# Kernel optimization log

Measured on AMD Instinct MI355X. Metric: run time of the kernel, lower is better.

## Reference

```python
import jax, jax.numpy as jnp
import numpy as np

K = 5  # top-k neighbors, from init kwarg

def setup_inputs() -> dict:
    key = jax.random.key(0)
    k1, k2 = jax.random.split(key)
    x = jax.random.normal(k1, (16384, 256), dtype=jnp.float32)
    reference_points = jax.random.normal(k2, (100, 256), dtype=jnp.float32)
    return {"x": x, "reference_points": reference_points}

def reference(x, reference_points):
    # Faithful to tf.norm(inputs[:,None] - ref[None], axis=-1):
    # materializes the [B, P, D] difference like the original, then L2 norm.
    diff = x[:, None, :] - reference_points[None, :, :]      # [B, P, D]
    distances = jnp.sqrt(jnp.sum(diff * diff, axis=-1))      # [B, P]
    # tf.math.top_k(-distances, k) -> indices of k smallest distances
    _, indices = jax.lax.top_k(-distances, K)                # [B, K] int32
    return indices
```

## Files before the change

kernel.cpp:

```cpp
#include <hip/hip_runtime.h>
#include <float.h>
#include <math.h>

#define NREF 100
#define NREF_PAD 128
#define DIM 256
#define K 5
#define ROWS 32
#define BLOCK 128
#define LDS_DW_REF 4096

__shared__ float lds_buf[20480];

__device__ __forceinline__ int swz(int dw) { return dw ^ ((dw >> 8) & 0x1C); }

__global__ __launch_bounds__(BLOCK, 1) void knn_kernel(
    const float* __restrict__ x, const float* __restrict__ ref,
    int* __restrict__ out, int nrows) {
#pragma clang fp contract(off)
  float* lds = lds_buf;
  const int tid = threadIdx.x;
  const int tx = tid & 15;
  const int ty = tid >> 4;
  const int RB = blockIdx.x * ROWS;

  float part[4][8], t01[4][8], t45[4][8], ae[4][8], ao[4][8];

  const int xlin0 = (4 * ty) * 128;
  const int rlin0 = LDS_DW_REF + (tx * 8) * 128;
  const int xkey = (xlin0 >> 8) & 0x1C;
  const int rkey = (rlin0 >> 8) & 0x1C;

#pragma unroll 1
  for (int c = 0; c < 2; c++) {
    const int DB = c * 128;
    if (c) __syncthreads();
#pragma unroll
    for (int k = 0; k < 8; k++) {
      const int idx = tid + k * BLOCK;
      const int row = idx >> 5, dp4 = idx & 31;
      float4 v = make_float4(0.f, 0.f, 0.f, 0.f);
      if (RB + row < nrows)
        v = *reinterpret_cast<const float4*>(x + (size_t)(RB + row) * DIM + DB + dp4 * 4);
      const int t = dp4 >> 1;
      const int jp0 = (dp4 & 1) << 1;
      const int dwA = row * 128 + jp0 * 32 + 2 * t;
      *reinterpret_cast<float2*>(&lds[swz(dwA)]) = make_float2(v.x, v.y);
      *reinterpret_cast<float2*>(&lds[swz(dwA + 32)]) = make_float2(v.z, v.w);
    }
#pragma unroll
    for (int k = 0; k < 32; k++) {
      const int idx = tid + k * BLOCK;
      const int r = idx >> 5, dp4 = idx & 31;
      if (r < NREF) {
        const float4 v = *reinterpret_cast<const float4*>(ref + (size_t)r * DIM + DB + dp4 * 4);
        const int t = dp4 >> 1;
        const int jp0 = (dp4 & 1) << 1;
        const int dwA = LDS_DW_REF + r * 128 + jp0 * 32 + 2 * t;
        *reinterpret_cast<float2*>(&lds[swz(dwA)]) = make_float2(v.x, v.y);
        *reinterpret_cast<float2*>(&lds[swz(dwA + 32)]) = make_float2(v.z, v.w);
      }
    }
    __syncthreads();

#pragma unroll
    for (int jp = 0; jp < 4; jp++) {
#pragma unroll
      for (int i = 0; i < 4; i++)
#pragma unroll
        for (int rr = 0; rr < 8; rr++) { ae[i][rr] = 0.f; ao[i][rr] = 0.f; }
#pragma unroll 1
      for (int tt = 0; tt < 8; tt++) {
        const int xa = (xlin0 + jp * 32) + ((4 * tt) ^ xkey);
        const int ra = (rlin0 + jp * 32) + ((4 * tt) ^ rkey);
        float4 xv[4], rv[8];
#pragma unroll
        for (int i = 0; i < 4; i++)
          xv[i] = *reinterpret_cast<const float4*>(&lds[xa + i * 128]);
#pragma unroll
        for (int rr = 0; rr < 8; rr++)
          rv[rr] = *reinterpret_cast<const float4*>(&lds[ra + rr * 128]);
#pragma unroll
        for (int i = 0; i < 4; i++)
#pragma unroll
          for (int rr = 0; rr < 8; rr++) {
            float d0 = xv[i].x - rv[rr].x; float s0 = d0 * d0; ae[i][rr] = ae[i][rr] + s0;
            float d1 = xv[i].z - rv[rr].z; float s1 = d1 * d1; ae[i][rr] = ae[i][rr] + s1;
            float d2 = xv[i].y - rv[rr].y; float s2 = d2 * d2; ao[i][rr] = ao[i][rr] + s2;
            float d3 = xv[i].w - rv[rr].w; float s3 = d3 * d3; ao[i][rr] = ao[i][rr] + s3;
          }
      }
#pragma unroll
      for (int i = 0; i < 4; i++)
#pragma unroll
        for (int rr = 0; rr < 8; rr++) {
          const float s = ae[i][rr] + ao[i][rr];
          if (jp == 0) t01[i][rr] = s;
          else if (jp == 1) t01[i][rr] = t01[i][rr] + s;
          else if (jp == 2) t45[i][rr] = s;
          else {
            t45[i][rr] = t45[i][rr] + s;
            const float blk = t01[i][rr] + t45[i][rr];
            part[i][rr] = c ? (part[i][rr] + blk) : blk;
          }
        }
    }
  }
  __syncthreads();
#pragma unroll
  for (int i = 0; i < 4; i++)
#pragma unroll
    for (int rr = 0; rr < 8; rr++)
      lds[(4 * ty + i) * 129 + tx * 8 + rr] = sqrtf(part[i][rr]);
  __syncthreads();
  if (tid < ROWS && RB + tid < nrows) {
    float best[K]; int bidx[K];
#pragma unroll
    for (int k = 0; k < K; k++) { best[k] = FLT_MAX; bidx[k] = 0; }
    for (int r = 0; r < NREF; r++) {
      const float kv = lds[tid * 129 + r];
      if (kv < best[K - 1]) {
        int pos = K - 1;
        while (pos > 0 && kv < best[pos - 1]) {
          best[pos] = best[pos - 1]; bidx[pos] = bidx[pos - 1]; pos--;
        }
        best[pos] = kv; bidx[pos] = r;
      }
    }
    int* o = out + (size_t)(RB + tid) * K;
#pragma unroll
    for (int k = 0; k < K; k++) o[k] = bidx[k];
  }
}

extern "C" void kernel_launch(void* const* d_in, const int* in_sizes, int n_in,
                              void* d_out, int out_size, void* d_ws, size_t ws_size,
                              hipStream_t stream) {
  const float* x = (const float*)d_in[0];
  const float* ref = (const float*)d_in[1];
  int* out = (int*)d_out;
  const int nrows = in_sizes[0] / DIM;
  const int grid = (nrows + ROWS - 1) / ROWS;
  knn_kernel<<<grid, BLOCK, 0, stream>>>(x, ref, out, nrows);
}
```

Measured before the change: 128.1 us.

## Halve rows per block, use padded 64-dim LDS chunks, raise occupancy

Rows per block go from 32 to 16, and the feature dimension is staged in four 64-wide chunks in a padded (stride 68) LDS layout. This replaces the XOR-swizzled 128-wide layout. Launch bounds now allow two blocks per SM, and the accumulation uses eight independent partial sums per output in place of the nested pair tree. The goal is more blocks and more latency hiding, at the cost of more barriers, reloading the reference set twice as often per row, and a changed summation order. Row-bounds checks on loads and on the final top-k were dropped, which assumes nrows is a multiple of 16.

Result: slower. 155.3 us (+21.2%).

```diff
diff --git a/kernel.cpp b/kernel.cpp
--- a/kernel.cpp
+++ b/kernel.cpp
@@ -3,122 +3,127 @@
 #include <math.h>
 
 #define NREF 100
-#define NREF_PAD 128
 #define DIM 256
 #define K 5
-#define ROWS 32
+#define ROWS 16
 #define BLOCK 128
-#define LDS_DW_REF 4096
+#define W 68
+#define REF_OFF (ROWS * W)
+#define NREFP 128
+#define LDS_DW (REF_OFF + NREFP * W)
 
-__shared__ float lds_buf[20480];
-
-__device__ __forceinline__ int swz(int dw) { return dw ^ ((dw >> 8) & 0x1C); }
-
-__global__ __launch_bounds__(BLOCK, 1) void knn_kernel(
+__global__ __launch_bounds__(BLOCK, 2) void knn_kernel(
     const float* __restrict__ x, const float* __restrict__ ref,
     int* __restrict__ out, int nrows) {
 #pragma clang fp contract(off)
-  float* lds = lds_buf;
+  __shared__ float lds[LDS_DW];
   const int tid = threadIdx.x;
   const int tx = tid & 15;
   const int ty = tid >> 4;
   const int RB = blockIdx.x * ROWS;
 
-  float part[4][8], t01[4][8], t45[4][8], ae[4][8], ao[4][8];
+  float acc[8][2][8];
+  float part[2][8];
+#pragma unroll
+  for (int q = 0; q < 8; q++)
+#pragma unroll
+    for (int i = 0; i < 2; i++)
+#pragma unroll
+      for (int rr = 0; rr < 8; rr++) acc[q][i][rr] = 0.f;
 
-  const int xlin0 = (4 * ty) * 128;
-  const int rlin0 = LDS_DW_REF + (tx * 8) * 128;
-  const int xkey = (xlin0 >> 8) & 0x1C;
-  const int rkey = (rlin0 >> 8) & 0x1C;
+  const float* xb = &lds[2 * ty * W];
+  const float* rb = &lds[REF_OFF + tx * W];
 
 #pragma unroll 1
-  for (int c = 0; c < 2; c++) {
-    const int DB = c * 128;
+  for (int c = 0; c < 4; c++) {
+    const int DB = c * 64;
     if (c) __syncthreads();
 #pragma unroll
-    for (int k = 0; k < 8; k++) {
+    for (int k = 0; k < 2; k++) {
       const int idx = tid + k * BLOCK;
-      const int row = idx >> 5, dp4 = idx & 31;
-      float4 v = make_float4(0.f, 0.f, 0.f, 0.f);
-      if (RB + row < nrows)
-        v = *reinterpret_cast<const float4*>(x + (size_t)(RB + row) * DIM + DB + dp4 * 4);
-      const int t = dp4 >> 1;
-      const int jp0 = (dp4 & 1) << 1;
-      const int dwA = row * 128 + jp0 * 32 + 2 * t;
-      *reinterpret_cast<float2*>(&lds[swz(dwA)]) = make_float2(v.x, v.y);
-      *reinterpret_cast<float2*>(&lds[swz(dwA + 32)]) = make_float2(v.z, v.w);
+      const int row = idx >> 4, dp = (idx & 15) << 2;
+      const float4 v = *reinterpret_cast<const float4*>(
+          x + (size_t)(RB + row) * DIM + DB + dp);
+      *reinterpret_cast<float4*>(&lds[row * W + dp]) = v;
     }
 #pragma unroll
-    for (int k = 0; k < 32; k++) {
+    for (int k = 0; k < 13; k++) {
       const int idx = tid + k * BLOCK;
-      const int r = idx >> 5, dp4 = idx & 31;
+      const int r = idx >> 4, dp = (idx & 15) << 2;
       if (r < NREF) {
-        const float4 v = *reinterpret_cast<const float4*>(ref + (size_t)r * DIM + DB + dp4 * 4);
-        const int t = dp4 >> 1;
-        const int jp0 = (dp4 & 1) << 1;
-        const int dwA = LDS_DW_REF + r * 128 + jp0 * 32 + 2 * t;
-        *reinterpret_cast<float2*>(&lds[swz(dwA)]) = make_float2(v.x, v.y);
-        *reinterpret_cast<float2*>(&lds[swz(dwA + 32)]) = make_float2(v.z, v.w);
+        const float4 v = *reinterpret_cast<const float4*>(
+            ref + (size_t)r * DIM + DB + dp);
+        *reinterpret_cast<float4*>(&lds[REF_OFF + r * W + dp]) = v;
       }
     }
     __syncthreads();
-
+#pragma unroll 2
+    for (int tt = 0; tt < 8; tt++) {
+      const int d0 = tt << 3;
+      {
+        float4 xv[2], rv[8];
 #pragma unroll
-    for (int jp = 0; jp < 4; jp++) {
-#pragma unroll
-      for (int i = 0; i < 4; i++)
-#pragma unroll
-        for (int rr = 0; rr < 8; rr++) { ae[i][rr] = 0.f; ao[i][rr] = 0.f; }
-#pragma unroll 1
-      for (int tt = 0; tt < 8; tt++) {
-        const int xa = (xlin0 + jp * 32) + ((4 * tt) ^ xkey);
-        const int ra = (rlin0 + jp * 32) + ((4 * tt) ^ rkey);
-        float4 xv[4], rv[8];
-#pragma unroll
-        for (int i = 0; i < 4; i++)
-          xv[i] = *reinterpret_cast<const float4*>(&lds[xa + i * 128]);
+        for (int i = 0; i < 2; i++)
+          xv[i] = *reinterpret_cast<const float4*>(xb + i * W + d0);
 #pragma unroll
         for (int rr = 0; rr < 8; rr++)
-          rv[rr] = *reinterpret_cast<const float4*>(&lds[ra + rr * 128]);
+          rv[rr] = *reinterpret_cast<const float4*>(rb + rr * 16 * W + d0);
 #pragma unroll
-        for (int i = 0; i < 4; i++)
+        for (int i = 0; i < 2; i++)
 #pragma unroll
           for (int rr = 0; rr < 8; rr++) {
-            float d0 = xv[i].x - rv[rr].x; float s0 = d0 * d0; ae[i][rr] = ae[i][rr] + s0;
-            float d1 = xv[i].z - rv[rr].z; float s1 = d1 * d1; ae[i][rr] = ae[i][rr] + s1;
-            float d2 = xv[i].y - rv[rr].y; float s2 = d2 * d2; ao[i][rr] = ao[i][rr] + s2;
-            float d3 = xv[i].w - rv[rr].w; float s3 = d3 * d3; ao[i][rr] = ao[i][rr] + s3;
+            float t0 = xv[i].x - rv[rr].x; float s0 = t0 * t0; acc[0][i][rr] = acc[0][i][rr] + s0;
+            float t1 = xv[i].y - rv[rr].y; float s1 = t1 * t1; acc[1][i][rr] = acc[1][i][rr] + s1;
+            float t2 = xv[i].z - rv[rr].z; float s2 = t2 * t2; acc[2][i][rr] = acc[2][i][rr] + s2;
+            float t3 = xv[i].w - rv[rr].w; float s3 = t3 * t3; acc[3][i][rr] = acc[3][i][rr] + s3;
           }
       }
+      {
+        float4 xv[2], rv[8];
 #pragma unroll
-      for (int i = 0; i < 4; i++)
+        for (int i = 0; i < 2; i++)
+          xv[i] = *reinterpret_cast<const float4*>(xb + i * W + d0 + 4);
+#pragma unroll
+        for (int rr = 0; rr < 8; rr++)
+          rv[rr] = *reinterpret_cast<const float4*>(rb + rr * 16 * W + d0 + 4);
+#pragma unroll
+        for (int i = 0; i < 2; i++)
+#pragma unroll
+          for (int rr = 0; rr < 8; rr++) {
+            float t0 = xv[i].x - rv[rr].x; float s0 = t0 * t0; acc[4][i][rr] = acc[4][i][rr] + s0;
+            float t1 = xv[i].y - rv[rr].y; float s1 = t1 * t1; acc[5][i][rr] = acc[5][i][rr] + s1;
+            float t2 = xv[i].z - rv[rr].z; float s2 = t2 * t2; acc[6][i][rr] = acc[6][i][rr] + s2;
+            float t3 = xv[i].w - rv[rr].w; float s3 = t3 * t3; acc[7][i][rr] = acc[7][i][rr] + s3;
+          }
+      }
+    }
+    if (c & 1) {
+#pragma unroll
+      for (int i = 0; i < 2; i++)
 #pragma unroll
         for (int rr = 0; rr < 8; rr++) {
-          const float s = ae[i][rr] + ao[i][rr];
-          if (jp == 0) t01[i][rr] = s;
-          else if (jp == 1) t01[i][rr] = t01[i][rr] + s;
-          else if (jp == 2) t45[i][rr] = s;
-          else {
-            t45[i][rr] = t45[i][rr] + s;
-            const float blk = t01[i][rr] + t45[i][rr];
-            part[i][rr] = c ? (part[i][rr] + blk) : blk;
-          }
+          const float s03 = (acc[0][i][rr] + acc[1][i][rr]) + (acc[2][i][rr] + acc[3][i][rr]);
+          const float s47 = (acc[4][i][rr] + acc[5][i][rr]) + (acc[6][i][rr] + acc[7][i][rr]);
+          const float blk = s03 + s47;
+          part[i][rr] = (c == 1) ? blk : (part[i][rr] + blk);
+#pragma unroll
+          for (int q = 0; q < 8; q++) acc[q][i][rr] = 0.f;
         }
     }
   }
   __syncthreads();
 #pragma unroll
-  for (int i = 0; i < 4; i++)
+  for (int i = 0; i < 2; i++)
 #pragma unroll
     for (int rr = 0; rr < 8; rr++)
-      lds[(4 * ty + i) * 129 + tx * 8 + rr] = sqrtf(part[i][rr]);
+      lds[(2 * ty + i) * 132 + tx + 16 * rr] = sqrtf(part[i][rr]);
   __syncthreads();
-  if (tid < ROWS && RB + tid < nrows) {
+  if (tid < ROWS) {
     float best[K]; int bidx[K];
 #pragma unroll
     for (int k = 0; k < K; k++) { best[k] = FLT_MAX; bidx[k] = 0; }
     for (int r = 0; r < NREF; r++) {
-      const float kv = lds[tid * 129 + r];
+      const float kv = lds[tid * 132 + r];
       if (kv < best[K - 1]) {
         int pos = K - 1;
         while (pos > 0 && kv < best[pos - 1]) {
```
